# Kernel tuning notes

Measured on AMD Instinct MI355X. Metric: run time of the kernel, lower is better.

Reference implementation:

```python
import jax, jax.numpy as jnp
import numpy as np

N, C, K, M = 100000, 128, 27, 4  # voxels, channels, 3^3 kernel offsets, branches
EPS = 1e-5


def setup_inputs() -> dict:
    key = jax.random.key(0)
    ks = jax.random.split(key, 4)
    x = jax.random.normal(ks[0], (N, C), jnp.float32)
    # neighbor index per voxel per kernel offset (Minkowski kernel map)
    nbr_idx = jax.random.randint(ks[1], (N, K), 0, N, dtype=jnp.int32)
    W1 = jax.random.normal(ks[2], (M, C, C), jnp.float32) * (1.0 / np.sqrt(C))
    g1 = jnp.ones((M, C), jnp.float32)
    b1 = jnp.zeros((M, C), jnp.float32)
    wk = jax.random.normal(ks[3], (M, K, C), jnp.float32) * (1.0 / np.sqrt(K))
    g_out = jnp.ones((C,), jnp.float32)
    b_out = jnp.zeros((C,), jnp.float32)
    return {"x": x, "nbr_idx": nbr_idx, "W1": W1, "g1": g1, "b1": b1,
            "wk": wk, "g_out": g_out, "b_out": b_out}


def _bn(h, g, b):
    # training-mode batch norm over the voxel axis
    mu = h.mean(0)
    var = h.var(0)
    return (h - mu) * jax.lax.rsqrt(var + EPS) * g + b


def reference(x, nbr_idx, W1, g1, b1, wk, g_out, b_out):
    out = jnp.zeros_like(x)
    for m in range(M):  # fixed small branch count
        # Conv1x1 (pointwise) + BN + ReLU
        h = jax.nn.relu(_bn(x @ W1[m], g1[m], b1[m]))  # [N, C]
        # channelwise 3^3 sparse conv: gather neighbor, per-channel scale, accumulate
        acc = jnp.zeros_like(h)
        for k in range(K):  # fixed 27 kernel offsets; avoids [N,K,C] materialization
            acc = acc + h[nbr_idx[:, k]] * wk[m, k]
        out = out + acc  # stack(-1).sum(-1) over branches
    out = jax.nn.relu(_bn(out, g_out, b_out))  # out_bn_relu
    out = out + x  # residual (inplanes == planes)
    return jax.nn.relu(out)  # final nonlinearity ('ReLU')
```

## Files before the change

kernel.cpp:

```cpp
#include <hip/hip_runtime.h>

#define KK 27
#define EPSV 1e-5f

typedef __attribute__((ext_vector_type(8))) short bf16x8;
typedef __attribute__((ext_vector_type(4))) float f32x4;
typedef __attribute__((ext_vector_type(4))) unsigned int u32x4;

static __device__ __forceinline__ unsigned short f2bf(float f) {
    unsigned u = __float_as_uint(f);
    u = u + 0x7fffu + ((u >> 16) & 1u);
    return (unsigned short)(u >> 16);
}

static __device__ __forceinline__ unsigned short f2h(float f) {
    _Float16 h = (_Float16)f;
    unsigned short u;
    __builtin_memcpy(&u, &h, 2);
    return u;
}
static __device__ __forceinline__ float h2f(unsigned short s) {
    _Float16 h;
    __builtin_memcpy(&h, &s, 2);
    return (float)h;
}
static __device__ __forceinline__ float hlo(unsigned u) { return h2f((unsigned short)(u & 0xffffu)); }
static __device__ __forceinline__ float hhi(unsigned u) { return h2f((unsigned short)(u >> 16)); }

__global__ void k0_wt(const float* __restrict__ W1, unsigned short* __restrict__ WT) {
    __shared__ unsigned short tile[128 * 18];
    const int m = blockIdx.x >> 3, n0 = (blockIdx.x & 7) * 16;
    const int t = threadIdx.x;
    const int kin = t >> 4, nin = t & 15;
#pragma unroll
    for (int it = 0; it < 8; ++it) {
        int k = it * 16 + kin;
        tile[k * 18 + nin] = f2bf(W1[((size_t)(m * 128 + k) * 128) + n0 + nin]);
    }
    __syncthreads();
    const int w = t >> 6, ko = (t & 63) * 2;
#pragma unroll
    for (int it = 0; it < 4; ++it) {
        int n = it * 4 + w;
        ushort2 v;
        v.x = tile[ko * 18 + n];
        v.y = tile[(ko + 1) * 18 + n];
        *(ushort2*)(WT + (size_t)(m * 128 + n0 + n) * 128 + ko) = v;
    }
}

__launch_bounds__(256)
__global__ void kA_gemm(const float* __restrict__ x, const unsigned short* __restrict__ WT,
                        unsigned short* __restrict__ Yall, float* __restrict__ ysum_b,
                        float* __restrict__ ysq_b, int binstride, int binmask,
                        int N, int m0, int m1, int ystride) {
    __shared__ unsigned short As[64 * 136];
    __shared__ unsigned short Bs[128 * 136];
    const int t = threadIdx.x;
    const int i0 = blockIdx.x * 64;
    const int binoff = (blockIdx.x & binmask) * binstride;

#pragma unroll
    for (int it = 0; it < 8; ++it) {
        int flat = it * 256 + t;
        int r = flat >> 5, c4 = (flat & 31) * 4;
        float4 v = make_float4(0.f, 0.f, 0.f, 0.f);
        if (i0 + r < N) v = *(const float4*)(x + (size_t)(i0 + r) * 128 + c4);
        ushort4 bb;
        bb.x = f2bf(v.x); bb.y = f2bf(v.y); bb.z = f2bf(v.z); bb.w = f2bf(v.w);
        *(ushort4*)(As + r * 136 + c4) = bb;
    }

    const int w = t >> 6, lane = t & 63;
    const int wr = w >> 1, wc = w & 1;
    const int r16 = lane & 15, q = lane >> 4;

    for (int m = m0; m < m1; ++m) {
        __syncthreads();
        const uint4* Wp = (const uint4*)(WT + (size_t)m * 128 * 128);
#pragma unroll
        for (int it = 0; it < 8; ++it) {
            int flat = it * 256 + t;
            int n = flat >> 4, kc = flat & 15;
            uint4 v = Wp[n * 16 + kc];
            *(uint4*)(Bs + n * 136 + kc * 8) = v;
        }
        __syncthreads();

        f32x4 acc[2][4];
#pragma unroll
        for (int a = 0; a < 2; ++a)
#pragma unroll
            for (int b = 0; b < 4; ++b) { acc[a][b][0] = 0.f; acc[a][b][1] = 0.f; acc[a][b][2] = 0.f; acc[a][b][3] = 0.f; }

#pragma unroll
        for (int ks = 0; ks < 4; ++ks) {
            int ko = ks * 32 + q * 8;
            bf16x8 af[2], bfr[4];
#pragma unroll
            for (int ri = 0; ri < 2; ++ri)
                af[ri] = *(const bf16x8*)(As + (wr * 32 + ri * 16 + r16) * 136 + ko);
#pragma unroll
            for (int ci = 0; ci < 4; ++ci)
                bfr[ci] = *(const bf16x8*)(Bs + (wc * 64 + ci * 16 + r16) * 136 + ko);
#pragma unroll
            for (int ri = 0; ri < 2; ++ri)
#pragma unroll
                for (int ci = 0; ci < 4; ++ci)
                    acc[ri][ci] = __builtin_amdgcn_mfma_f32_16x16x32_bf16(af[ri], bfr[ci], acc[ri][ci], 0, 0, 0);
        }

#pragma unroll
        for (int ci = 0; ci < 4; ++ci) {
            float s = 0.f, s2 = 0.f;
#pragma unroll
            for (int ri = 0; ri < 2; ++ri) {
#pragma unroll
                for (int r = 0; r < 4; ++r) {
                    int row = i0 + wr * 32 + ri * 16 + q * 4 + r;
                    float vv = acc[ri][ci][r];
                    if (row < N) { s += vv; s2 += vv * vv; }
                }
            }
            s  += __shfl_xor(s, 16);  s  += __shfl_xor(s, 32);
            s2 += __shfl_xor(s2, 16); s2 += __shfl_xor(s2, 32);
            if (lane < 16) {
                int col = wc * 64 + ci * 16 + r16;
                atomicAdd(ysum_b + binoff + m * 128 + col, s);
                atomicAdd(ysq_b  + binoff + m * 128 + col, s2);
            }
        }

        __syncthreads();
        unsigned short* Ys = Bs;
#pragma unroll
        for (int ci = 0; ci < 4; ++ci) {
            int col = wc * 64 + ci * 16 + r16;
#pragma unroll
            for (int ri = 0; ri < 2; ++ri) {
#pragma unroll
                for (int r = 0; r < 4; ++r) {
                    int rl = wr * 32 + ri * 16 + q * 4 + r;
                    Ys[rl * 136 + col] = f2h(acc[ri][ci][r]);
                }
            }
        }
        __syncthreads();
        const int cb = (m - m0) * 128;
#pragma unroll
        for (int it = 0; it < 4; ++it) {
            int chunk = it * 256 + t;
            int row = chunk >> 4, c8 = (chunk & 15) * 8;
            if (i0 + row < N) {
                u32x4 v = *(const u32x4*)(Ys + row * 136 + c8);
                __builtin_nontemporal_store(v, (u32x4*)(Yall + (size_t)(i0 + row) * ystride + cb + c8));
            }
        }
    }
}

__global__ void k2_coef_b(const float* __restrict__ ysum_b, const float* __restrict__ ysq_b,
                          int nbin, int binstride,
                          const float* __restrict__ g1, const float* __restrict__ b1,
                          float* __restrict__ a1, float* __restrict__ c1, int N) {
    int idx = blockIdx.x * blockDim.x + threadIdx.x;
    float s = 0.f, s2 = 0.f;
    for (int b = 0; b < nbin; ++b) {
        s  += ysum_b[b * binstride + idx];
        s2 += ysq_b [b * binstride + idx];
    }
    float mean = s / (float)N;
    float var  = s2 / (float)N - mean * mean;
    float a = g1[idx] * rsqrtf(var + EPSV);
    a1[idx] = a;
    c1[idx] = b1[idx] - mean * a;
}

__global__ void k2_coef(const float* __restrict__ ysum, const float* __restrict__ ysq,
                        const float* __restrict__ g1, const float* __restrict__ b1,
                        float* __restrict__ a1, float* __restrict__ c1, int N, int m0) {
    int c = threadIdx.x & 127;
    int m = m0 + (threadIdx.x >> 7);
    float mean = ysum[m * 128 + c] / (float)N;
    float var  = ysq[m * 128 + c] / (float)N - mean * mean;
    float a = g1[m * 128 + c] * rsqrtf(var + EPSV);
    a1[m * 128 + c] = a;
    c1[m * 128 + c] = b1[m * 128 + c] - mean * a;
}

__launch_bounds__(256)
__global__ void k4_all(const unsigned short* __restrict__ Y, const int* __restrict__ nbr,
                       const float* __restrict__ wkg, const float* __restrict__ A1g,
                       const float* __restrict__ C1g, float* __restrict__ P,
                       float* __restrict__ osum_b, float* __restrict__ osq_b, int N) {
    __shared__ unsigned short wkL[4 * KK * 136];
    __shared__ float ssum[128], ssq[128];
    const int t = threadIdx.x;
    for (int idx = t; idx < 4 * KK * 128; idx += 256) {
        int c = idx & 127, km = idx >> 7;
        wkL[km * 136 + c] = f2h(wkg[idx]);
    }
    if (t < 128) { ssum[t] = 0.f; ssq[t] = 0.f; }

    const int lane = t & 63;
    const int m = lane >> 4, c16 = lane & 15;
    const int q = m;
    const unsigned short* wbase = wkL + (m * KK) * 136 + c16 * 8;
    const unsigned short* hbase = Y + lane * 8;

    float Ar[8], Cr[8];
    {
        const float4 A0 = *(const float4*)(A1g + m * 128 + c16 * 8);
        const float4 A1 = *(const float4*)(A1g + m * 128 + c16 * 8 + 4);
        const float4 C0 = *(const float4*)(C1g + m * 128 + c16 * 8);
        const float4 C1 = *(const float4*)(C1g + m * 128 + c16 * 8 + 4);
        Ar[0]=A0.x; Ar[1]=A0.y; Ar[2]=A0.z; Ar[3]=A0.w;
        Ar[4]=A1.x; Ar[5]=A1.y; Ar[6]=A1.z; Ar[7]=A1.w;
        Cr[0]=C0.x; Cr[1]=C0.y; Cr[2]=C0.z; Cr[3]=C0.w;
        Cr[4]=C1.x; Cr[5]=C1.y; Cr[6]=C1.z; Cr[7]=C1.w;
    }
    __syncthreads();

    float os[8], oq[8];
#pragma unroll
    for (int e = 0; e < 8; ++e) { os[e] = 0.f; oq[e] = 0.f; }

    const int wid = blockIdx.x * 4 + (t >> 6);
    const int nw  = gridDim.x * 4;
    const int ng  = (N + 3) >> 2;
    for (int vg = wid; vg < ng; vg += nw) {
        const int v0 = __builtin_amdgcn_readfirstlane(vg << 2);
        const int* np = nbr + (size_t)v0 * KK;
        const int o1 = (v0 + 1 < N) ? KK : 0;
        const int o2 = (v0 + 2 < N) ? 2 * KK : 0;
        const int o3 = (v0 + 3 < N) ? 3 * KK : 0;
        float acc0[8], acc1[8], acc2[8], acc3[8];
#pragma unroll
        for (int e = 0; e < 8; ++e) { acc0[e] = 0.f; acc1[e] = 0.f; acc2[e] = 0.f; acc3[e] = 0.f; }

#pragma unroll 3
        for (int k = 0; k < KK; ++k) {
            const int j0 = np[k];
            const int j1 = np[o1 + k];
            const int j2 = np[o2 + k];
            const int j3 = np[o3 + k];
            const uint4 hv0 = *(const uint4*)(hbase + ((size_t)j0 << 9));
            const uint4 hv1 = *(const uint4*)(hbase + ((size_t)j1 << 9));
            const uint4 hv2 = *(const uint4*)(hbase + ((size_t)j2 << 9));
            const uint4 hv3 = *(const uint4*)(hbase + ((size_t)j3 << 9));
            const uint4 wv  = *(const uint4*)(wbase + k * 136);
            const float w0 = hlo(wv.x), w1 = hhi(wv.x), w2 = hlo(wv.y), w3 = hhi(wv.y);
            const float w4 = hlo(wv.z), w5 = hhi(wv.z), w6 = hlo(wv.w), w7 = hhi(wv.w);
#define K4BODY(A, H)                                                        \
            A[0] += fmaxf(0.f, hlo(H.x) * Ar[0] + Cr[0]) * w0;              \
            A[1] += fmaxf(0.f, hhi(H.x) * Ar[1] + Cr[1]) * w1;              \
            A[2] += fmaxf(0.f, hlo(H.y) * Ar[2] + Cr[2]) * w2;              \
            A[3] += fmaxf(0.f, hhi(H.y) * Ar[3] + Cr[3]) * w3;              \
            A[4] += fmaxf(0.f, hlo(H.z) * Ar[4] + Cr[4]) * w4;              \
            A[5] += fmaxf(0.f, hhi(H.z) * Ar[5] + Cr[5]) * w5;              \
            A[6] += fmaxf(0.f, hlo(H.w) * Ar[6] + Cr[6]) * w6;              \
            A[7] += fmaxf(0.f, hhi(H.w) * Ar[7] + Cr[7]) * w7;
            K4BODY(acc0, hv0)
            K4BODY(acc1, hv1)
            K4BODY(acc2, hv2)
            K4BODY(acc3, hv3)
#undef K4BODY
        }

#pragma unroll
        for (int e = 0; e < 8; ++e) {
            acc0[e] += __shfl_xor(acc0[e], 16); acc0[e] += __shfl_xor(acc0[e], 32);
            acc1[e] += __shfl_xor(acc1[e], 16); acc1[e] += __shfl_xor(acc1[e], 32);
            acc2[e] += __shfl_xor(acc2[e], 16); acc2[e] += __shfl_xor(acc2[e], 32);
            acc3[e] += __shfl_xor(acc3[e], 16); acc3[e] += __shfl_xor(acc3[e], 32);
        }
        float av[8];
#pragma unroll
        for (int e = 0; e < 8; ++e)
            av[e] = (q == 0) ? acc0[e] : (q == 1) ? acc1[e] : (q == 2) ? acc2[e] : acc3[e];
        const int vq = v0 + q;
        if (vq < N) {
            f32x4 x0 = {av[0], av[1], av[2], av[3]};
            f32x4 x1 = {av[4], av[5], av[6], av[7]};
            float* p = P + (size_t)vq * 128 + c16 * 8;
            __builtin_nontemporal_store(x0, (f32x4*)p);
            __builtin_nontemporal_store(x1, (f32x4*)(p + 4));
#pragma unroll
            for (int e = 0; e < 8; ++e) { os[e] += av[e]; oq[e] += av[e] * av[e]; }
        }
    }

#pragma unroll
    for (int e = 0; e < 8; ++e) {
        atomicAdd(ssum + c16 * 8 + e, os[e]);
        atomicAdd(ssq  + c16 * 8 + e, oq[e]);
    }
    __syncthreads();
    if (t < 128) {
        const int bo = (blockIdx.x & 3) * 128;
        atomicAdd(osum_b + bo + t, ssum[t]);
        atomicAdd(osq_b  + bo + t, ssq[t]);
    }
}

template <int MODE>
__launch_bounds__(256)
__global__ void k4_gather(const unsigned short* __restrict__ Ym, int ystride,
                          const int* __restrict__ nbr,
                          const float* __restrict__ wkm, const float* __restrict__ a1m,
                          const float* __restrict__ c1m, float* __restrict__ P,
                          float* __restrict__ osum, float* __restrict__ osq, int N) {
    __shared__ float wkL[KK * 132];
    __shared__ float ssum[128], ssq[128];
    const int t = threadIdx.x;
    for (int idx = t; idx < KK * 128; idx += 256) {
        int k = idx >> 7, c = idx & 127;
        wkL[k * 132 + c] = wkm[k * 128 + c];
    }
    if (MODE == 2) { if (t < 128) { ssum[t] = 0.f; ssq[t] = 0.f; } }

    const int w = t >> 6, lane = t & 63;
    const int q = lane >> 4, c16 = lane & 15;
    const int slot = w * 4 + q;
    const int vox = blockIdx.x * 16 + slot;
    const bool alive = vox < N;

    float aR[8], cR[8];
    {
        const float4 A0 = *(const float4*)(a1m + c16 * 8);
        const float4 A1 = *(const float4*)(a1m + c16 * 8 + 4);
        const float4 C0 = *(const float4*)(c1m + c16 * 8);
        const float4 C1 = *(const float4*)(c1m + c16 * 8 + 4);
        aR[0]=A0.x; aR[1]=A0.y; aR[2]=A0.z; aR[3]=A0.w;
        aR[4]=A1.x; aR[5]=A1.y; aR[6]=A1.z; aR[7]=A1.w;
        cR[0]=C0.x; cR[1]=C0.y; cR[2]=C0.z; cR[3]=C0.w;
        cR[4]=C1.x; cR[5]=C1.y; cR[6]=C1.z; cR[7]=C1.w;
    }
    __syncthreads();

    const long long base = alive ? (long long)vox * KK : 0;
    float acc[8];
#pragma unroll
    for (int e = 0; e < 8; ++e) acc[e] = 0.f;

#pragma unroll 3
    for (int k = 0; k < KK; ++k) {
        int j = nbr[base + k];
        const uint4 hv = *(const uint4*)(Ym + (size_t)j * ystride + c16 * 8);
        const float4 wa = *(const float4*)(wkL + k * 132 + c16 * 8);
        const float4 wb = *(const float4*)(wkL + k * 132 + c16 * 8 + 4);
        float h0 = fmaxf(0.f, hlo(hv.x) * aR[0] + cR[0]);
        float h1 = fmaxf(0.f, hhi(hv.x) * aR[1] + cR[1]);
        float h2 = fmaxf(0.f, hlo(hv.y) * aR[2] + cR[2]);
        float h3 = fmaxf(0.f, hhi(hv.y) * aR[3] + cR[3]);
        float h4 = fmaxf(0.f, hlo(hv.z) * aR[4] + cR[4]);
        float h5 = fmaxf(0.f, hhi(hv.z) * aR[5] + cR[5]);
        float h6 = fmaxf(0.f, hlo(hv.w) * aR[6] + cR[6]);
        float h7 = fmaxf(0.f, hhi(hv.w) * aR[7] + cR[7]);
        acc[0] += h0 * wa.x; acc[1] += h1 * wa.y;
        acc[2] += h2 * wa.z; acc[3] += h3 * wa.w;
        acc[4] += h4 * wb.x; acc[5] += h5 * wb.y;
        acc[6] += h6 * wb.z; acc[7] += h7 * wb.w;
    }

    float os[8], oq[8];
    if (alive) {
        float* p = P + (size_t)vox * 128 + c16 * 8;
        if (MODE == 0) {
            float4 v0 = {acc[0], acc[1], acc[2], acc[3]};
            float4 v1 = {acc[4], acc[5], acc[6], acc[7]};
            *(float4*)p = v0;
            *(float4*)(p + 4) = v1;
        } else {
            float4 o0 = *(const float4*)p, o1 = *(const float4*)(p + 4);
            o0.x += acc[0]; o0.y += acc[1]; o0.z += acc[2]; o0.w += acc[3];
            o1.x += acc[4]; o1.y += acc[5]; o1.z += acc[6]; o1.w += acc[7];
            *(float4*)p = o0;
            *(float4*)(p + 4) = o1;
            if (MODE == 2) {
                os[0] = o0.x; oq[0] = o0.x * o0.x;
                os[1] = o0.y; oq[1] = o0.y * o0.y;
                os[2] = o0.z; oq[2] = o0.z * o0.z;
                os[3] = o0.w; oq[3] = o0.w * o0.w;
                os[4] = o1.x; oq[4] = o1.x * o1.x;
                os[5] = o1.y; oq[5] = o1.y * o1.y;
                os[6] = o1.z; oq[6] = o1.z * o1.z;
                os[7] = o1.w; oq[7] = o1.w * o1.w;
            }
        }
    }
    if (MODE == 2) {
        if (!alive) {
#pragma unroll
            for (int e = 0; e < 8; ++e) { os[e] = 0.f; oq[e] = 0.f; }
        }
#pragma unroll
        for (int e = 0; e < 8; ++e) {
            os[e] += __shfl_xor(os[e], 16); os[e] += __shfl_xor(os[e], 32);
            oq[e] += __shfl_xor(oq[e], 16); oq[e] += __shfl_xor(oq[e], 32);
        }
        if (lane < 16) {
#pragma unroll
            for (int e = 0; e < 8; ++e) {
                atomicAdd(ssum + c16 * 8 + e, os[e]);
                atomicAdd(ssq  + c16 * 8 + e, oq[e]);
            }
        }
        __syncthreads();
        if (t < 128) {
            atomicAdd(osum + t, ssum[t]);
            atomicAdd(osq  + t, ssq[t]);
        }
    }
}

__global__ void k5_coef(const float* __restrict__ osum_b, const float* __restrict__ osq_b,
                        int nbin,
                        const float* __restrict__ g, const float* __restrict__ b,
                        float* __restrict__ ao, float* __restrict__ co, int N) {
    int c = threadIdx.x;
    float s = 0.f, s2 = 0.f;
    for (int bi = 0; bi < nbin; ++bi) {
        s  += osum_b[bi * 128 + c];
        s2 += osq_b [bi * 128 + c];
    }
    float mean = s / (float)N;
    float var  = s2 / (float)N - mean * mean;
    float a = g[c] * rsqrtf(var + EPSV);
    ao[c] = a;
    co[c] = b[c] - mean * a;
}

__launch_bounds__(256)
__global__ void k6_final(float* __restrict__ P, const float* __restrict__ x,
                         const float* __restrict__ ao, const float* __restrict__ co, int N) {
    long long t4 = ((long long)blockIdx.x * 256 + threadIdx.x) * 4;
    if (t4 >= (long long)N * 128) return;
    int c4 = (int)(t4 & 127);
    float4 p  = *(const float4*)(P + t4);
    float4 xv = *(const float4*)(x + t4);
    float4 a  = *(const float4*)(ao + c4);
    float4 c  = *(const float4*)(co + c4);
    float4 o;
    o.x = fmaxf(0.f, fmaxf(0.f, p.x * a.x + c.x) + xv.x);
    o.y = fmaxf(0.f, fmaxf(0.f, p.y * a.y + c.y) + xv.y);
    o.z = fmaxf(0.f, fmaxf(0.f, p.z * a.z + c.z) + xv.z);
    o.w = fmaxf(0.f, fmaxf(0.f, p.w * a.w + c.w) + xv.w);
    *(float4*)(P + t4) = o;
}

extern "C" void kernel_launch(void* const* d_in, const int* in_sizes, int n_in,
                              void* d_out, int out_size, void* d_ws, size_t ws_size,
                              hipStream_t stream) {
    const float* x     = (const float*)d_in[0];
    const int*   nbr   = (const int*)d_in[1];
    const float* W1    = (const float*)d_in[2];
    const float* g1    = (const float*)d_in[3];
    const float* b1    = (const float*)d_in[4];
    const float* wk    = (const float*)d_in[5];
    const float* g_out = (const float*)d_in[6];
    const float* b_out = (const float*)d_in[7];
    const int N = in_sizes[0] / 128;

    float* P = (float*)d_out;
    char* ws = (char*)d_ws;
    float* ysum = (float*)ws;
    float* ysq  = ysum + 512;
    float* osum = ysq + 512;
    float* osq  = osum + 128;
    float* osb  = osq + 128;
    float* oqb  = osb + 512;
    float* a1   = oqb + 512;
    float* c1   = a1 + 512;
    float* ao   = c1 + 512;
    float* co   = ao + 128;
    unsigned short* WT = (unsigned short*)(ws + 16384);
    unsigned short* Y  = (unsigned short*)(ws + 16384 + 131072);

    const bool fused = ws_size >= (size_t)16384 + 131072 + (size_t)N * 512 * 2;

    hipMemsetAsync(d_ws, 0, 16384, stream);
    k0_wt<<<32, 256, 0, stream>>>(W1, WT);

    const int gA = (N + 63) / 64;
    const int g4 = (N + 15) / 16;

    if (fused) {
        float* ysum_b = P;
        float* ysq_b  = P + 64 * 512;
        hipMemsetAsync(d_out, 0, 64 * 512 * 2 * sizeof(float), stream);
        kA_gemm<<<gA, 256, 0, stream>>>(x, WT, Y, ysum_b, ysq_b, 512, 63, N, 0, 4, 512);
        k2_coef_b<<<2, 256, 0, stream>>>(ysum_b, ysq_b, 64, 512, g1, b1, a1, c1, N);
        k4_all<<<2048, 256, 0, stream>>>(Y, nbr, wk, a1, c1, P, osb, oqb, N);
        k5_coef<<<1, 128, 0, stream>>>(osb, oqb, 4, g_out, b_out, ao, co, N);
    } else {
        for (int m = 0; m < 4; ++m) {
            kA_gemm<<<gA, 256, 0, stream>>>(x, WT, Y, ysum, ysq, 0, 0, N, m, m + 1, 128);
            k2_coef<<<1, 128, 0, stream>>>(ysum, ysq, g1, b1, a1, c1, N, m);
            if (m == 0)
                k4_gather<0><<<g4, 256, 0, stream>>>(Y, 128, nbr, wk + m * KK * 128,
                                                     a1 + m * 128, c1 + m * 128, P, osum, osq, N);
            else if (m == 3)
                k4_gather<2><<<g4, 256, 0, stream>>>(Y, 128, nbr, wk + m * KK * 128,
                                                     a1 + m * 128, c1 + m * 128, P, osum, osq, N);
            else
                k4_gather<1><<<g4, 256, 0, stream>>>(Y, 128, nbr, wk + m * KK * 128,
                                                     a1 + m * 128, c1 + m * 128, P, osum, osq, N);
        }
        k5_coef<<<1, 128, 0, stream>>>(osum, osq, 1, g_out, b_out, ao, co, N);
    }
    const int g6 = (int)(((long long)N * 128 / 4 + 255) / 256);
    k6_final<<<g6, 256, 0, stream>>>(P, x, ao, co, N);
}
```

Before: 588.1 us.

## Fold memsets into weight-transpose kernel, fuse BN coef into final kernel, enlarge GEMM tile

After: 598.5 us. About the same (+1.8%).

```diff
diff --git a/kernel.cpp b/kernel.cpp
--- a/kernel.cpp
+++ b/kernel.cpp
@@ -27,10 +27,15 @@
 static __device__ __forceinline__ float hlo(unsigned u) { return h2f((unsigned short)(u & 0xffffu)); }
 static __device__ __forceinline__ float hhi(unsigned u) { return h2f((unsigned short)(u >> 16)); }
 
-__global__ void k0_wt(const float* __restrict__ W1, unsigned short* __restrict__ WT) {
+__global__ void k0_wt(const float* __restrict__ W1, unsigned short* __restrict__ WT,
+                      float* __restrict__ z1, int n1, float* __restrict__ z2, int n2) {
+    const int t = threadIdx.x;
+    const int gt = blockIdx.x * 256 + t;
+    for (int i = gt; i < n1; i += 32 * 256) z1[i] = 0.f;
+    for (int i = gt; i < n2; i += 32 * 256) z2[i] = 0.f;
+
     __shared__ unsigned short tile[128 * 18];
     const int m = blockIdx.x >> 3, n0 = (blockIdx.x & 7) * 16;
-    const int t = threadIdx.x;
     const int kin = t >> 4, nin = t & 15;
 #pragma unroll
     for (int it = 0; it < 8; ++it) {
@@ -54,14 +59,14 @@
                         unsigned short* __restrict__ Yall, float* __restrict__ ysum_b,
                         float* __restrict__ ysq_b, int binstride, int binmask,
                         int N, int m0, int m1, int ystride) {
-    __shared__ unsigned short As[64 * 136];
+    __shared__ unsigned short As[128 * 136];
     __shared__ unsigned short Bs[128 * 136];
     const int t = threadIdx.x;
-    const int i0 = blockIdx.x * 64;
+    const int i0 = blockIdx.x * 128;
     const int binoff = (blockIdx.x & binmask) * binstride;
 
 #pragma unroll
-    for (int it = 0; it < 8; ++it) {
+    for (int it = 0; it < 16; ++it) {
         int flat = it * 256 + t;
         int r = flat >> 5, c4 = (flat & 31) * 4;
         float4 v = make_float4(0.f, 0.f, 0.f, 0.f);
@@ -72,7 +77,6 @@
     }
 
     const int w = t >> 6, lane = t & 63;
-    const int wr = w >> 1, wc = w & 1;
     const int r16 = lane & 15, q = lane >> 4;
 
     for (int m = m0; m < m1; ++m) {
@@ -87,37 +91,37 @@
         }
         __syncthreads();
 
-        f32x4 acc[2][4];
+        f32x4 acc[2][8];
 #pragma unroll
         for (int a = 0; a < 2; ++a)
 #pragma unroll
-            for (int b = 0; b < 4; ++b) { acc[a][b][0] = 0.f; acc[a][b][1] = 0.f; acc[a][b][2] = 0.f; acc[a][b][3] = 0.f; }
+            for (int b = 0; b < 8; ++b) { acc[a][b][0] = 0.f; acc[a][b][1] = 0.f; acc[a][b][2] = 0.f; acc[a][b][3] = 0.f; }
 
 #pragma unroll
         for (int ks = 0; ks < 4; ++ks) {
             int ko = ks * 32 + q * 8;
-            bf16x8 af[2], bfr[4];
+            bf16x8 af[2], bfr[8];
 #pragma unroll
             for (int ri = 0; ri < 2; ++ri)
-                af[ri] = *(const bf16x8*)(As + (wr * 32 + ri * 16 + r16) * 136 + ko);
-#pragma unroll
-            for (int ci = 0; ci < 4; ++ci)
-                bfr[ci] = *(const bf16x8*)(Bs + (wc * 64 + ci * 16 + r16) * 136 + ko);
+                af[ri] = *(const bf16x8*)(As + (w * 32 + ri * 16 + r16) * 136 + ko);
+#pragma unroll
+            for (int ci = 0; ci < 8; ++ci)
+                bfr[ci] = *(const bf16x8*)(Bs + (ci * 16 + r16) * 136 + ko);
 #pragma unroll
             for (int ri = 0; ri < 2; ++ri)
 #pragma unroll
-                for (int ci = 0; ci < 4; ++ci)
+                for (int ci = 0; ci < 8; ++ci)
                     acc[ri][ci] = __builtin_amdgcn_mfma_f32_16x16x32_bf16(af[ri], bfr[ci], acc[ri][ci], 0, 0, 0);
         }
 
 #pragma unroll
-        for (int ci = 0; ci < 4; ++ci) {
+        for (int ci = 0; ci < 8; ++ci) {
             float s = 0.f, s2 = 0.f;
 #pragma unroll
             for (int ri = 0; ri < 2; ++ri) {
 #pragma unroll
                 for (int r = 0; r < 4; ++r) {
-                    int row = i0 + wr * 32 + ri * 16 + q * 4 + r;
+                    int row = i0 + w * 32 + ri * 16 + q * 4 + r;
                     float vv = acc[ri][ci][r];
                     if (row < N) { s += vv; s2 += vv * vv; }
                 }
@@ -125,7 +129,7 @@
             s  += __shfl_xor(s, 16);  s  += __shfl_xor(s, 32);
             s2 += __shfl_xor(s2, 16); s2 += __shfl_xor(s2, 32);
             if (lane < 16) {
-                int col = wc * 64 + ci * 16 + r16;
+                int col = ci * 16 + r16;
                 atomicAdd(ysum_b + binoff + m * 128 + col, s);
                 atomicAdd(ysq_b  + binoff + m * 128 + col, s2);
             }
@@ -134,13 +138,13 @@
         __syncthreads();
         unsigned short* Ys = Bs;
 #pragma unroll
-        for (int ci = 0; ci < 4; ++ci) {
-            int col = wc * 64 + ci * 16 + r16;
+        for (int ci = 0; ci < 8; ++ci) {
+            int col = ci * 16 + r16;
 #pragma unroll
             for (int ri = 0; ri < 2; ++ri) {
 #pragma unroll
                 for (int r = 0; r < 4; ++r) {
-                    int rl = wr * 32 + ri * 16 + q * 4 + r;
+                    int rl = w * 32 + ri * 16 + q * 4 + r;
                     Ys[rl * 136 + col] = f2h(acc[ri][ci][r]);
                 }
             }
@@ -148,7 +152,7 @@
         __syncthreads();
         const int cb = (m - m0) * 128;
 #pragma unroll
-        for (int it = 0; it < 4; ++it) {
+        for (int it = 0; it < 8; ++it) {
             int chunk = it * 256 + t;
             int row = chunk >> 4, c8 = (chunk & 15) * 8;
             if (i0 + row < N) {
@@ -174,18 +178,6 @@
     float a = g1[idx] * rsqrtf(var + EPSV);
     a1[idx] = a;
     c1[idx] = b1[idx] - mean * a;
-}
-
-__global__ void k2_coef(const float* __restrict__ ysum, const float* __restrict__ ysq,
-                        const float* __restrict__ g1, const float* __restrict__ b1,
-                        float* __restrict__ a1, float* __restrict__ c1, int N, int m0) {
-    int c = threadIdx.x & 127;
-    int m = m0 + (threadIdx.x >> 7);
-    float mean = ysum[m * 128 + c] / (float)N;
-    float var  = ysq[m * 128 + c] / (float)N - mean * mean;
-    float a = g1[m * 128 + c] * rsqrtf(var + EPSV);
-    a1[m * 128 + c] = a;
-    c1[m * 128 + c] = b1[m * 128 + c] - mean * a;
 }
 
 __launch_bounds__(256)
@@ -414,38 +406,36 @@
     }
 }
 
-__global__ void k5_coef(const float* __restrict__ osum_b, const float* __restrict__ osq_b,
-                        int nbin,
-                        const float* __restrict__ g, const float* __restrict__ b,
-                        float* __restrict__ ao, float* __restrict__ co, int N) {
-    int c = threadIdx.x;
-    float s = 0.f, s2 = 0.f;
-    for (int bi = 0; bi < nbin; ++bi) {
-        s  += osum_b[bi * 128 + c];
-        s2 += osq_b [bi * 128 + c];
-    }
-    float mean = s / (float)N;
-    float var  = s2 / (float)N - mean * mean;
-    float a = g[c] * rsqrtf(var + EPSV);
-    ao[c] = a;
-    co[c] = b[c] - mean * a;
-}
-
 __launch_bounds__(256)
 __global__ void k6_final(float* __restrict__ P, const float* __restrict__ x,
-                         const float* __restrict__ ao, const float* __restrict__ co, int N) {
-    long long t4 = ((long long)blockIdx.x * 256 + threadIdx.x) * 4;
+                         const float* __restrict__ osum_b, const float* __restrict__ osq_b,
+                         int nbin, const float* __restrict__ g, const float* __restrict__ b,
+                         int N) {
+    __shared__ float aoS[128], coS[128];
+    const int t = threadIdx.x;
+    if (t < 128) {
+        float s = 0.f, s2 = 0.f;
+        for (int bi = 0; bi < nbin; ++bi) {
+            s  += osum_b[bi * 128 + t];
+            s2 += osq_b [bi * 128 + t];
+        }
+        float mean = s / (float)N;
+        float var  = s2 / (float)N - mean * mean;
+        float a = g[t] * rsqrtf(var + EPSV);
+        aoS[t] = a;
+        coS[t] = b[t] - mean * a;
+    }
+    __syncthreads();
+    long long t4 = ((long long)blockIdx.x * 256 + t) * 4;
     if (t4 >= (long long)N * 128) return;
     int c4 = (int)(t4 & 127);
     float4 p  = *(const float4*)(P + t4);
     float4 xv = *(const float4*)(x + t4);
-    float4 a  = *(const float4*)(ao + c4);
-    float4 c  = *(const float4*)(co + c4);
     float4 o;
-    o.x = fmaxf(0.f, fmaxf(0.f, p.x * a.x + c.x) + xv.x);
-    o.y = fmaxf(0.f, fmaxf(0.f, p.y * a.y + c.y) + xv.y);
-    o.z = fmaxf(0.f, fmaxf(0.f, p.z * a.z + c.z) + xv.z);
-    o.w = fmaxf(0.f, fmaxf(0.f, p.w * a.w + c.w) + xv.w);
+    o.x = fmaxf(0.f, fmaxf(0.f, p.x * aoS[c4 + 0] + coS[c4 + 0]) + xv.x);
+    o.y = fmaxf(0.f, fmaxf(0.f, p.y * aoS[c4 + 1] + coS[c4 + 1]) + xv.y);
+    o.z = fmaxf(0.f, fmaxf(0.f, p.z * aoS[c4 + 2] + coS[c4 + 2]) + xv.z);
+    o.w = fmaxf(0.f, fmaxf(0.f, p.w * aoS[c4 + 3] + coS[c4 + 3]) + xv.w);
     *(float4*)(P + t4) = o;
 }
 
@@ -472,31 +462,31 @@
     float* oqb  = osb + 512;
     float* a1   = oqb + 512;
     float* c1   = a1 + 512;
-    float* ao   = c1 + 512;
-    float* co   = ao + 128;
     unsigned short* WT = (unsigned short*)(ws + 16384);
     unsigned short* Y  = (unsigned short*)(ws + 16384 + 131072);
 
     const bool fused = ws_size >= (size_t)16384 + 131072 + (size_t)N * 512 * 2;
 
-    hipMemsetAsync(d_ws, 0, 16384, stream);
-    k0_wt<<<32, 256, 0, stream>>>(W1, WT);
-
-    const int gA = (N + 63) / 64;
+    const int gA = (N + 127) / 128;
     const int g4 = (N + 15) / 16;
+    const int g6 = (int)(((long long)N * 128 / 4 + 255) / 256);
 
     if (fused) {
         float* ysum_b = P;
         float* ysq_b  = P + 64 * 512;
-        hipMemsetAsync(d_out, 0, 64 * 512 * 2 * sizeof(float), stream);
+        k0_wt<<<32, 256, 0, stream>>>(W1, WT, ysum_b, 64 * 512 * 2, osb, 1024);
         kA_gemm<<<gA, 256, 0, stream>>>(x, WT, Y, ysum_b, ysq_b, 512, 63, N, 0, 4, 512);
         k2_coef_b<<<2, 256, 0, stream>>>(ysum_b, ysq_b, 64, 512, g1, b1, a1, c1, N);
         k4_all<<<2048, 256, 0, stream>>>(Y, nbr, wk, a1, c1, P, osb, oqb, N);
-        k5_coef<<<1, 128, 0, stream>>>(osb, oqb, 4, g_out, b_out, ao, co, N);
+        k6_final<<<g6, 256, 0, stream>>>(P, x, osb, oqb, 4, g_out, b_out, N);
     } else {
+        hipMemsetAsync(d_ws, 0, 16384, stream);
+        k0_wt<<<32, 256, 0, stream>>>(W1, WT, nullptr, 0, nullptr, 0);
         for (int m = 0; m < 4; ++m) {
             kA_gemm<<<gA, 256, 0, stream>>>(x, WT, Y, ysum, ysq, 0, 0, N, m, m + 1, 128);
-            k2_coef<<<1, 128, 0, stream>>>(ysum, ysq, g1, b1, a1, c1, N, m);
+            k2_coef_b<<<1, 128, 0, stream>>>(ysum + m * 128, ysq + m * 128, 1, 0,
+                                             g1 + m * 128, b1 + m * 128,
+                                             a1 + m * 128, c1 + m * 128, N);
             if (m == 0)
                 k4_gather<0><<<g4, 256, 0, stream>>>(Y, 128, nbr, wk + m * KK * 128,
                                                      a1 + m * 128, c1 + m * 128, P, osum, osq, N);
@@ -507,8 +497,6 @@
                 k4_gather<1><<<g4, 256, 0, stream>>>(Y, 128, nbr, wk + m * KK * 128,
                                                      a1 + m * 128, c1 + m * 128, P, osum, osq, N);
         }
-        k5_coef<<<1, 128, 0, stream>>>(osum, osq, 1, g_out, b_out, ao, co, N);
-    }
-    const int g6 = (int)(((long long)N * 128 / 4 + 255) / 256);
-    k6_final<<<g6, 256, 0, stream>>>(P, x, ao, co, N);
-}
+        k6_final<<<g6, 256, 0, stream>>>(P, x, osum, osq, 1, g_out, b_out, N);
+    }
+}
```
